# Performance work log

Hardware: AMD Instinct MI355X
Metric: run time of the kernel (lower is better)

Reference implementation:

```python
import jax, jax.numpy as jnp
import numpy as np

N_HASHES = 4
CHUNK = 144
REDUCTION = 4
RES_SCALE = 1.0
NORM_EPS = 5e-5


def conv2d(x, w, b, pad):
    y = jax.lax.conv_general_dilated(
        x, w, window_strides=(1, 1), padding=[(pad, pad), (pad, pad)],
        dimension_numbers=('NCHW', 'OIHW', 'NCHW'))
    return y + b[None, :, None, None]


def add_adjacent_buckets(x):
    # x: (N, h, n_chunks, chunk, e); concat each chunk with its circular neighbors
    back = jnp.roll(x, 1, axis=2)
    fwd = jnp.roll(x, -1, axis=2)
    return jnp.concatenate([x, back, fwd], axis=3)


def setup_inputs() -> dict:
    key = jax.random.key(0)
    ks = jax.random.split(key, 6)
    x = jax.random.normal(ks[0], (1, 32, 192, 192), jnp.float32)
    w_match = jax.random.normal(ks[1], (8, 32, 3, 3), jnp.float32) * 0.05
    b_match = jnp.zeros((8,), jnp.float32)
    w_asm = jax.random.normal(ks[2], (32, 32, 1, 1), jnp.float32) * 0.05
    b_asm = jnp.zeros((32,), jnp.float32)
    rotations = jax.random.normal(ks[3], (8, N_HASHES, 64), jnp.float32)
    return {'x': x, 'w_match': w_match, 'b_match': b_match,
            'w_asm': w_asm, 'b_asm': b_asm, 'rotations': rotations}


def reference(x, w_match, b_match, w_asm, b_asm, rotations):
    N, _, H, W = x.shape
    L = H * W
    # conv_match: 3x3 conv 32->8; conv_assembly: 1x1 conv 32->32
    x_embed = conv2d(x, w_match, b_match, 1).reshape(N, -1, L).transpose(0, 2, 1)  # (N, L, 8)
    y_embed = conv2d(x, w_asm, b_asm, 0).reshape(N, -1, L).transpose(0, 2, 1)      # (N, L, 32)
    C = x_embed.shape[-1]
    hash_buckets = min(L // CHUNK + (L // CHUNK) % 2, 128)  # = 128 here

    # --- LSH hashing (non-differentiable; rotations passed in for determinism) ---
    rotated = jnp.einsum('blf,fhi->bhli', x_embed, rotations)        # (N, h, L, hb/2)
    rotated = jnp.concatenate([rotated, -rotated], axis=-1)          # (N, h, L, hb)
    hash_codes = jnp.argmax(rotated, axis=-1)                        # (N, h, L)
    hash_codes = hash_codes + (jnp.arange(N_HASHES) * hash_buckets)[None, :, None]
    hash_codes = hash_codes.reshape(N, -1)                           # (N, h*L)

    # --- sort tokens by bucket id ---
    indices = jnp.argsort(hash_codes, axis=-1)
    undo_sort = jnp.argsort(indices, axis=-1)
    mod_indices = indices % L
    x_sorted = jnp.take_along_axis(x_embed, mod_indices[:, :, None], axis=1)  # (N, h*L, 8)
    y_sorted = jnp.take_along_axis(y_embed, mod_indices[:, :, None], axis=1)  # (N, h*L, 32)

    x_b = x_sorted.reshape(N, N_HASHES, -1, C)
    y_b = y_sorted.reshape(N, N_HASHES, -1, C * REDUCTION)
    padding = (-L) % CHUNK  # static; 0 for L=192*192
    if padding:
        x_b = jnp.concatenate([x_b, x_b[:, :, -padding:, :]], axis=2)
        y_b = jnp.concatenate([y_b, y_b[:, :, -padding:, :]], axis=2)
    x_b = x_b.reshape(N, N_HASHES, -1, CHUNK, C)
    y_b = y_b.reshape(N, N_HASHES, -1, CHUNK, C * REDUCTION)

    # --- bucketed attention with adjacent buckets ---
    nrm = jnp.linalg.norm(x_b, axis=-1, keepdims=True)
    x_match = x_b / jnp.maximum(nrm, NORM_EPS)   # F.normalize(eps=5e-5)
    x_match = add_adjacent_buckets(x_match)      # (N, h, k, 3*chunk, 8)
    y_adj = add_adjacent_buckets(y_b)            # (N, h, k, 3*chunk, 32)

    raw = jnp.einsum('bhkie,bhkje->bhkij', x_b, x_match)  # (N, h, k, 144, 432)
    bucket_score = jax.scipy.special.logsumexp(raw, axis=-1, keepdims=True)
    score = jnp.exp(raw - bucket_score)
    ret = jnp.einsum('bhkij,bhkje->bhkie', score, y_adj)  # (N, h, k, 144, 32)

    ret = ret.reshape(N, N_HASHES, -1, C * REDUCTION)
    bucket_score = bucket_score.reshape(N, N_HASHES, -1)
    if padding:
        ret = ret[:, :, :-padding, :]
        bucket_score = bucket_score[:, :, :-padding]
    ret = ret.reshape(N, -1, C * REDUCTION)
    bucket_score = bucket_score.reshape(N, -1)

    # --- unsort and combine hash rounds via softmax over logsumexp scores ---
    ret = jnp.take_along_axis(ret, undo_sort[:, :, None], axis=1)
    bucket_score = jnp.take_along_axis(bucket_score, undo_sort, axis=1)
    ret = ret.reshape(N, N_HASHES, L, C * REDUCTION)
    probs = jax.nn.softmax(bucket_score.reshape(N, N_HASHES, L, 1), axis=1)
    out = jnp.sum(ret * probs, axis=1)                     # (N, L, 32)
    out = out.transpose(0, 2, 1).reshape(N, -1, H, W) * RES_SCALE + x
    return out
```

## Files before the change

### kernel.cpp

```cpp
#include <hip/hip_runtime.h>
#include <hip/hip_bf16.h>
#include <math.h>

#define LTOT 36864
#define NH 4
#define NCHUNK 256
#define CHU 144
#define NBUCK 128
#define NSEG 144
#define HW_ 192
#define VTS 148

typedef unsigned int u32;
typedef unsigned short u16;
typedef unsigned long long u64;
typedef __attribute__((ext_vector_type(4))) short short4v;
typedef __attribute__((ext_vector_type(4))) float f32x4;

__device__ __forceinline__ u32 pkbf(float a, float b){
  union { __hip_bfloat162 h2; u32 u; } cv;
  cv.h2 = __float22bfloat162_rn(float2{a,b});
  return cv.u;
}
__device__ __forceinline__ float bflo(u32 w){ return __uint_as_float(w<<16); }
__device__ __forceinline__ float bfhi(u32 w){ return __uint_as_float(w & 0xffff0000u); }

__global__ __launch_bounds__(256) void k_conv(const float* __restrict__ x,
    const float* __restrict__ wm, const float* __restrict__ bm,
    const float* __restrict__ wa, const float* __restrict__ ba,
    float* __restrict__ xe, u16* __restrict__ Vu)
{
  __shared__ float xs[32*108];
  const int t = threadIdx.x;
  const int id = blockIdx.x;
  const int bx = id % 12, by = id / 12;

  for (int idx=t; idx<3456; idx+=256){
    int ci = idx/108, rem = idx-ci*108;
    int iy = rem/18,  ix = rem-iy*18;
    int yy = by*4+iy-1, xx = bx*16+ix-1;
    float v = 0.f;
    if (yy>=0 && yy<HW_ && xx>=0 && xx<HW_) v = x[ci*LTOT + yy*HW_ + xx];
    xs[idx] = v;
  }
  __syncthreads();
  const int lane = t & 63;
  const int w  = __builtin_amdgcn_readfirstlane(t>>6);
  const int co0 = 2*w, cb = 8*w;
  const int ix = lane & 15, iy = lane >> 4;
  float a0 = bm[co0], a1 = bm[co0+1];
  float acc[8];
  #pragma unroll
  for (int co=0;co<8;co++) acc[co] = ba[cb+co];
  const float* xb  = xs + iy*18 + ix;
  const float* w0p = wm + co0*288;
  const float* w1p = w0p + 288;
  for (int ci=0; ci<32; ci++){
    const float* xp = xb + ci*108;
    float x00=xp[0],  x01=xp[1],  x02=xp[2];
    float x10=xp[18], x11=xp[19], x12=xp[20];
    float x20=xp[36], x21=xp[37], x22=xp[38];
    const float* w0 = w0p + ci*9;
    const float* w1 = w1p + ci*9;
    a0 += x00*w0[0]+x01*w0[1]+x02*w0[2]
        + x10*w0[3]+x11*w0[4]+x12*w0[5]
        + x20*w0[6]+x21*w0[7]+x22*w0[8];
    a1 += x00*w1[0]+x01*w1[1]+x02*w1[2]
        + x10*w1[3]+x11*w1[4]+x12*w1[5]
        + x20*w1[6]+x21*w1[7]+x22*w1[8];
    const float* wap = wa + cb*32 + ci;
    #pragma unroll
    for (int co=0;co<8;co++) acc[co] += x11 * wap[co*32];
  }
  const int l = (by*4+iy)*HW_ + bx*16+ix;
  *(float2*)(xe + l*8 + co0) = float2{a0,a1};
  uint4 vv;
  vv.x = pkbf(acc[0],acc[1]); vv.y = pkbf(acc[2],acc[3]);
  vv.z = pkbf(acc[4],acc[5]); vv.w = pkbf(acc[6],acc[7]);
  *(uint4*)(Vu + (size_t)l*32 + cb) = vv;
}

__global__ __launch_bounds__(256) void k_hashrank(const float* __restrict__ xe,
    const float* __restrict__ rot, int* __restrict__ code,
    int* __restrict__ lrank, int* __restrict__ hist)
{
  const int h = blockIdx.y, seg = blockIdx.x, t = threadIdx.x;
  const int l = seg*256 + t;
  const float4* qp = (const float4*)(xe + l*8);
  float4 qa = qp[0], qb = qp[1];
  float best = -INFINITY; int bi = 0;
  float worst = INFINITY; int wi = 0;
  for (int i=0; i<64; i++){
    const float* rp = rot + h*64 + i;
    float v = qa.x*rp[0]    + qa.y*rp[256]  + qa.z*rp[512]  + qa.w*rp[768]
            + qb.x*rp[1024] + qb.y*rp[1280] + qb.z*rp[1536] + qb.w*rp[1792];
    if (v > best)  { best  = v; bi = i; }
    if (v < worst) { worst = v; wi = i; }
  }
  int c = (-worst > best) ? (64+wi) : bi;
  code[h*LTOT + l] = c;

  const int lane = t & 63, w = t >> 6;
  u64 mask = ~0ull;
  #pragma unroll
  for (int bit=0; bit<7; bit++){
    u64 bset = __ballot((c>>bit)&1);
    mask &= ((c>>bit)&1) ? bset : ~bset;
  }
  int rin = __popcll(mask & ((lane==0)?0ull:(~0ull >> (64-lane))));
  int cnt = __popcll(mask);

  __shared__ int wh[4][NBUCK];
  ((int*)wh)[t] = 0; ((int*)wh)[t+256] = 0;
  __syncthreads();
  if (rin == 0) wh[w][c] = cnt;
  __syncthreads();
  int r = rin;
  for (int ww=0; ww<w; ww++) r += wh[ww][c];
  lrank[h*LTOT + l] = r;
  if (t < NBUCK) hist[(h*NSEG+seg)*NBUCK + t] = wh[0][t]+wh[1][t]+wh[2][t]+wh[3][t];
}

__global__ __launch_bounds__(512) void k_scan(const int* __restrict__ hist,
    int* __restrict__ segoff)
{
  const int h = blockIdx.x;
  const int b = threadIdx.x & 127, g = threadIdx.x >> 7;
  int vals[36];
  int sum = 0;
  #pragma unroll
  for (int i=0;i<36;i++){
    vals[i] = hist[(h*NSEG + g*36 + i)*NBUCK + b];
    sum += vals[i];
  }
  __shared__ int ps[4][NBUCK];
  __shared__ int tot[NBUCK];
  __shared__ int scv[NBUCK];
  ps[g][b] = sum;
  __syncthreads();
  if (g == 0){
    int run = 0;
    #pragma unroll
    for (int gg=0; gg<4; gg++){ int tv = ps[gg][b]; ps[gg][b] = run; run += tv; }
    tot[b] = run;
    int v = run;
    #pragma unroll
    for (int off=1; off<64; off<<=1){
      int u = __shfl_up(v, off);
      if ((b & 63) >= off) v += u;
    }
    scv[b] = v;
  }
  __syncthreads();
  int base = scv[b] - tot[b] + ((b >= 64) ? scv[63] : 0);
  int run2 = base + ps[g][b];
  #pragma unroll
  for (int i=0;i<36;i++){
    segoff[(h*NSEG + g*36 + i)*NBUCK + b] = run2;
    run2 += vals[i];
  }
}

__global__ __launch_bounds__(256) void k_scatter(const int* __restrict__ code,
    const int* __restrict__ lrank, const int* __restrict__ segoff,
    const float* __restrict__ xe, const u16* __restrict__ Vu,
    int* __restrict__ spos, u16* __restrict__ Ks, u16* __restrict__ Qs,
    u16* __restrict__ Vs)
{
  const int h = blockIdx.y, seg = blockIdx.x, t = threadIdx.x;
  const int l = seg*256 + t;
  int c = code[h*LTOT + l];
  int r = segoff[(h*NSEG+seg)*NBUCK + c] + lrank[h*LTOT + l];
  spos[h*LTOT + r] = l;

  const float4* xr = (const float4*)(xe + l*8);
  float4 a = xr[0], b = xr[1];
  float n2 = a.x*a.x+a.y*a.y+a.z*a.z+a.w*a.w
           + b.x*b.x+b.y*b.y+b.z*b.z+b.w*b.w;
  float sc = 1.0f / fmaxf(sqrtf(n2), 5e-5f);
  uint4 kk, qq;
  kk.x = pkbf(a.x*sc,a.y*sc); kk.y = pkbf(a.z*sc,a.w*sc);
  kk.z = pkbf(b.x*sc,b.y*sc); kk.w = pkbf(b.z*sc,b.w*sc);
  qq.x = pkbf(a.x,a.y); qq.y = pkbf(a.z,a.w);
  qq.z = pkbf(b.x,b.y); qq.w = pkbf(b.z,b.w);
  *(uint4*)(Ks + (size_t)(h*LTOT + r)*8) = kk;
  *(uint4*)(Qs + (size_t)(h*LTOT + r)*8) = qq;

  const uint4* vr = (const uint4*)(Vu + (size_t)l*32);
  uint4* vp = (uint4*)(Vs + (size_t)(h*LTOT + r)*32);
  vp[0] = vr[0]; vp[1] = vr[1]; vp[2] = vr[2]; vp[3] = vr[3];
}

__global__ __launch_bounds__(320) void k_attn(const u16* __restrict__ Ks,
    const u16* __restrict__ Qs, const u16* __restrict__ Vs,
    const int* __restrict__ spos, u16* __restrict__ ret_u, float* __restrict__ bs_u)
{
  __shared__ __align__(16) u16 Klds[CHU*8];
  __shared__ __align__(16) u16 Qlds[CHU*8];
  __shared__ __align__(16) u16 VT[32*VTS];
  __shared__ float qn[CHU];
  __shared__ int spos_l[CHU];

  const int t = threadIdx.x;
  const int k = blockIdx.x, h = blockIdx.y;

  if (t < CHU){
    uint4 qv = *(const uint4*)(Qs + (size_t)(h*LTOT + k*CHU + t)*8);
    *(uint4*)(Qlds + t*8) = qv;
    float f0=bflo(qv.x), f1=bfhi(qv.x), f2=bflo(qv.y), f3=bfhi(qv.y);
    float f4=bflo(qv.z), f5=bfhi(qv.z), f6=bflo(qv.w), f7=bfhi(qv.w);
    qn[t] = sqrtf(f0*f0+f1*f1+f2*f2+f3*f3+f4*f4+f5*f5+f6*f6+f7*f7)*1.01f + 1e-6f;
    spos_l[t] = spos[h*LTOT + k*CHU + t];
  }
  __syncthreads();

  const int lane = t & 63;
  const int wv = t >> 6;
  const int q = lane & 15;
  const int quad = lane >> 4;
  const bool two = (wv < 4);
  const int tl0 = 2*wv;
  const int tl1 = two ? (2*wv+1) : 8;

  const short4v zs = {0,0,0,0};
  short4v bq0 = zs, bq1 = zs;
  if (quad < 2){
    bq0 = *(const short4v*)(Qlds + (tl0*16+q)*8 + quad*4);
    if (two) bq1 = *(const short4v*)(Qlds + (tl1*16+q)*8 + quad*4);
  }
  const float m0 = qn[tl0*16+q];
  const float m1 = two ? qn[tl1*16+q] : 0.f;

  f32x4 o00={0,0,0,0}, o01={0,0,0,0}, o10={0,0,0,0}, o11={0,0,0,0};
  float s0 = 0.f, s1 = 0.f;

  for (int r=0; r<3; r++){
    __syncthreads();
    const int gkb = ((k + NCHUNK-1 + r) & (NCHUNK-1)) * CHU;
    if (t < CHU){
      *(uint4*)(Klds + t*8) = *(const uint4*)(Ks + (size_t)(h*LTOT + gkb + t)*8);
    } else if (t >= 176){
      int i = t - 176;
      int p = i >> 1, hf = i & 1;
      const uint4* ra = (const uint4*)(Vs + (size_t)(h*LTOT + gkb + 2*p)*32);
      const uint4* rb = (const uint4*)(Vs + (size_t)(h*LTOT + gkb + 2*p+1)*32);
      uint4 A0 = ra[hf*2], A1 = ra[hf*2+1];
      uint4 B0 = rb[hf*2], B1 = rb[hf*2+1];
      u32 aw[8] = {A0.x,A0.y,A0.z,A0.w,A1.x,A1.y,A1.z,A1.w};
      u32 bw[8] = {B0.x,B0.y,B0.z,B0.w,B1.x,B1.y,B1.z,B1.w};
      int ebase = hf*16;
      #pragma unroll
      for (int m=0;m<8;m++){
        u32 al = aw[m]&0xffffu, ah = aw[m]>>16;
        u32 bl = bw[m]&0xffffu, bh = bw[m]>>16;
        *(u32*)&VT[(ebase+2*m  )*VTS + 2*p] = al | (bl<<16);
        *(u32*)&VT[(ebase+2*m+1)*VTS + 2*p] = ah | (bh<<16);
      }
    }
    __syncthreads();

    #pragma unroll 3
    for (int kt=0; kt<9; kt++){
      short4v av = zs;
      if (quad < 2) av = *(const short4v*)(Klds + (kt*16+q)*8 + quad*4);
      f32x4 zc = {0.f,0.f,0.f,0.f};
      f32x4 stA = __builtin_amdgcn_mfma_f32_16x16x16bf16_1k(av, bq0, zc, 0,0,0);

      float pA0 = __expf(stA[0]-m0), pA1 = __expf(stA[1]-m0);
      float pA2 = __expf(stA[2]-m0), pA3 = __expf(stA[3]-m0);
      s0 += (pA0+pA1)+(pA2+pA3);
      union { u32 u[2]; short4v s4; } pkA;
      pkA.u[0] = pkbf(pA0,pA1); pkA.u[1] = pkbf(pA2,pA3);

      short4v va0 = *(const short4v*)(&VT[ q    *VTS + kt*16 + quad*4]);
      short4v va1 = *(const short4v*)(&VT[(q+16)*VTS + kt*16 + quad*4]);
      o00 = __builtin_amdgcn_mfma_f32_16x16x16bf16_1k(va0, pkA.s4, o00, 0,0,0);
      o01 = __builtin_amdgcn_mfma_f32_16x16x16bf16_1k(va1, pkA.s4, o01, 0,0,0);

      if (two){
        f32x4 stB = __builtin_amdgcn_mfma_f32_16x16x16bf16_1k(av, bq1, zc, 0,0,0);
        float pB0 = __expf(stB[0]-m1), pB1 = __expf(stB[1]-m1);
        float pB2 = __expf(stB[2]-m1), pB3 = __expf(stB[3]-m1);
        s1 += (pB0+pB1)+(pB2+pB3);
        union { u32 u[2]; short4v s4; } pkB;
        pkB.u[0] = pkbf(pB0,pB1); pkB.u[1] = pkbf(pB2,pB3);
        o10 = __builtin_amdgcn_mfma_f32_16x16x16bf16_1k(va0, pkB.s4, o10, 0,0,0);
        o11 = __builtin_amdgcn_mfma_f32_16x16x16bf16_1k(va1, pkB.s4, o11, 0,0,0);
      }
    }
  }

  float st0 = s0;
  st0 += __shfl_xor(st0, 16); st0 += __shfl_xor(st0, 32);
  float inv0 = 1.0f/st0;

  const int pos0 = spos_l[tl0*16 + q];
  u16* rp0 = ret_u + (size_t)(h*LTOT + pos0)*32;
  uint2 wA, wB;
  wA.x = pkbf(o00[0]*inv0, o00[1]*inv0); wA.y = pkbf(o00[2]*inv0, o00[3]*inv0);
  wB.x = pkbf(o01[0]*inv0, o01[1]*inv0); wB.y = pkbf(o01[2]*inv0, o01[3]*inv0);
  *(uint2*)&rp0[quad*4]    = wA;
  *(uint2*)&rp0[16+quad*4] = wB;
  if (quad == 0) bs_u[h*LTOT + pos0] = m0 + __logf(st0);

  if (two){
    float st1 = s1;
    st1 += __shfl_xor(st1, 16); st1 += __shfl_xor(st1, 32);
    float inv1 = 1.0f/st1;
    const int pos1 = spos_l[tl1*16 + q];
    u16* rp1 = ret_u + (size_t)(h*LTOT + pos1)*32;
    wA.x = pkbf(o10[0]*inv1, o10[1]*inv1); wA.y = pkbf(o10[2]*inv1, o10[3]*inv1);
    wB.x = pkbf(o11[0]*inv1, o11[1]*inv1); wB.y = pkbf(o11[2]*inv1, o11[3]*inv1);
    *(uint2*)&rp1[quad*4]    = wA;
    *(uint2*)&rp1[16+quad*4] = wB;
    if (quad == 0) bs_u[h*LTOT + pos1] = m1 + __logf(st1);
  }
}

__global__ __launch_bounds__(256) void k_final(const float* __restrict__ x,
    const u16* __restrict__ ret_u, const float* __restrict__ bs_u,
    float* __restrict__ out)
{
  const int l  = blockIdx.x*64 + (threadIdx.x & 63);
  const int eg = threadIdx.x >> 6;
  float bs[NH];
  #pragma unroll
  for (int h=0;h<NH;h++) bs[h] = bs_u[h*LTOT + l];
  float m = fmaxf(fmaxf(bs[0],bs[1]), fmaxf(bs[2],bs[3]));
  float p[NH]; float s = 0.f;
  #pragma unroll
  for (int h=0;h<NH;h++){ p[h] = __expf(bs[h]-m); s += p[h]; }
  float inv = 1.0f/s;
  float o[8];
  #pragma unroll
  for (int e=0;e<8;e++) o[e]=0.f;
  #pragma unroll
  for (int h=0;h<NH;h++){
    float w = p[h]*inv;
    uint4 v = *(const uint4*)(ret_u + (size_t)(h*LTOT + l)*32 + eg*8);
    o[0] += w*bflo(v.x); o[1] += w*bfhi(v.x);
    o[2] += w*bflo(v.y); o[3] += w*bfhi(v.y);
    o[4] += w*bflo(v.z); o[5] += w*bfhi(v.z);
    o[6] += w*bflo(v.w); o[7] += w*bfhi(v.w);
  }
  #pragma unroll
  for (int e=0;e<8;e++){
    int ge = eg*8 + e;
    out[ge*LTOT + l] = o[e] + x[ge*LTOT + l];
  }
}

extern "C" void kernel_launch(void* const* d_in, const int* in_sizes, int n_in,
                              void* d_out, int out_size, void* d_ws, size_t ws_size,
                              hipStream_t stream)
{
  const float* x   = (const float*)d_in[0];
  const float* wm  = (const float*)d_in[1];
  const float* bm  = (const float*)d_in[2];
  const float* wa  = (const float*)d_in[3];
  const float* ba  = (const float*)d_in[4];
  const float* rot = (const float*)d_in[5];
  float* out = (float*)d_out;

  char* ws = (char*)d_ws;
  size_t off = 0;
  auto alloc = [&](size_t bytes)->void*{
    void* p = ws + off;
    off = (off + bytes + 255) & ~(size_t)255;
    return p;
  };
  float* xe     = (float*)alloc((size_t)LTOT*8*4);
  u16*   Vu     = (u16*)  alloc((size_t)LTOT*32*2);
  int*   code   = (int*)  alloc((size_t)NH*LTOT*4);
  int*   lrank  = (int*)  alloc((size_t)NH*LTOT*4);
  int*   hist   = (int*)  alloc((size_t)NH*NSEG*NBUCK*4);
  int*   segoff = (int*)  alloc((size_t)NH*NSEG*NBUCK*4);
  int*   spos   = (int*)  alloc((size_t)NH*LTOT*4);
  u16*   Ks     = (u16*)  alloc((size_t)NH*LTOT*8*2);
  u16*   Qs     = (u16*)  alloc((size_t)NH*LTOT*8*2);
  u16*   Vs     = (u16*)  alloc((size_t)NH*LTOT*32*2);
  u16*   ret_u  = (u16*)  alloc((size_t)NH*LTOT*32*2);
  float* bs_u   = (float*)alloc((size_t)NH*LTOT*4);

  hipLaunchKernelGGL(k_conv,     dim3(576),        dim3(256), 0, stream, x, wm, bm, wa, ba, xe, Vu);
  hipLaunchKernelGGL(k_hashrank, dim3(NSEG,NH),    dim3(256), 0, stream, xe, rot, code, lrank, hist);
  hipLaunchKernelGGL(k_scan,     dim3(NH),         dim3(512), 0, stream, hist, segoff);
  hipLaunchKernelGGL(k_scatter,  dim3(NSEG,NH),    dim3(256), 0, stream, code, lrank, segoff, xe, Vu, spos, Ks, Qs, Vs);
  hipLaunchKernelGGL(k_attn,     dim3(NCHUNK,NH),  dim3(320), 0, stream, Ks, Qs, Vs, spos, ret_u, bs_u);
  hipLaunchKernelGGL(k_final,    dim3(576),        dim3(256), 0, stream, x, ret_u, bs_u, out);
}
```

Measured before the change: 130.5 us.

## Preload all neighbour K chunks and double-buffer V with register prefetch

All three adjacent K chunks are now loaded into a larger shared buffer once at kernel start, so K no longer has to be reloaded each round. V tiles use two shared buffers: the next chunk's V is fetched into registers before the MFMA loop and transposed into the other buffer afterwards. This drops from two barriers per round to one and overlaps global V loads with compute. The cost is more shared memory and extra live registers for the prefetched V. A stray no-op read-modify-write on VT remains in the prologue.

```diff
diff --git a/kernel.cpp b/kernel.cpp
--- a/kernel.cpp
+++ b/kernel.cpp
@@ -195,14 +195,17 @@
     const u16* __restrict__ Qs, const u16* __restrict__ Vs,
     const int* __restrict__ spos, u16* __restrict__ ret_u, float* __restrict__ bs_u)
 {
-  __shared__ __align__(16) u16 Klds[CHU*8];
+  __shared__ __align__(16) u16 Klds[432*8];
   __shared__ __align__(16) u16 Qlds[CHU*8];
-  __shared__ __align__(16) u16 VT[32*VTS];
+  __shared__ __align__(16) u16 VT[2][32*VTS];
   __shared__ float qn[CHU];
   __shared__ int spos_l[CHU];
 
   const int t = threadIdx.x;
   const int k = blockIdx.x, h = blockIdx.y;
+  const int vp_i = t - 176, vp_p = vp_i >> 1, vp_hf = vp_i & 1;
+
+  uint4 vpa0, vpa1, vpb0, vpb1;
 
   if (t < CHU){
     uint4 qv = *(const uint4*)(Qs + (size_t)(h*LTOT + k*CHU + t)*8);
@@ -211,6 +214,31 @@
     float f4=bflo(qv.z), f5=bfhi(qv.z), f6=bflo(qv.w), f7=bfhi(qv.w);
     qn[t] = sqrtf(f0*f0+f1*f1+f2*f2+f3*f3+f4*f4+f5*f5+f6*f6+f7*f7)*1.01f + 1e-6f;
     spos_l[t] = spos[h*LTOT + k*CHU + t];
+    #pragma unroll
+    for (int rr=0; rr<3; rr++){
+      const int gkb = ((k + NCHUNK-1 + rr) & (NCHUNK-1)) * CHU;
+      *(uint4*)(Klds + (rr*CHU + t)*8) =
+          *(const uint4*)(Ks + (size_t)(h*LTOT + gkb + t)*8);
+    }
+  } else if (t >= 176){
+    const int gkb = ((k + NCHUNK-1) & (NCHUNK-1)) * CHU;
+    const uint4* ra = (const uint4*)(Vs + (size_t)(h*LTOT + gkb + 2*vp_p)*32);
+    const uint4* rb = (const uint4*)(Vs + (size_t)(h*LTOT + gkb + 2*vp_p+1)*32);
+    vpa0 = ra[vp_hf*2]; vpa1 = ra[vp_hf*2+1];
+    vpb0 = rb[vp_hf*2]; vpb1 = rb[vp_hf*2+1];
+  }
+  if (t >= 176){
+    u32 aw[8] = {vpa0.x,vpa0.y,vpa0.z,vpa0.w,vpa1.x,vpa1.y,vpa1.z,vpa1.w};
+    u32 bw[8] = {vpb0.x,vpb0.y,vpb0.z,vpb0.w,vpb1.x,vpb1.y,vpb1.z,vpb1.w};
+    int ebase = vp_hf*16;
+    #pragma unroll
+    for (int m=0;m<8;m++){
+      u32 al = aw[m]&0xffffu, ah = aw[m]>>16;
+      u32 bl = bw[m]&0xffffu, bh = bw[m]>>16;
+      VT[0][(ebase+2*m  )*VTS + 2*vp_p] |= 0;
+      *(u32*)&VT[0][(ebase+2*m  )*VTS + 2*vp_p] = al | (bl<<16);
+      *(u32*)&VT[0][(ebase+2*m+1)*VTS + 2*vp_p] = ah | (bh<<16);
+    }
   }
   __syncthreads();
 
@@ -235,34 +263,19 @@
   float s0 = 0.f, s1 = 0.f;
 
   for (int r=0; r<3; r++){
-    __syncthreads();
-    const int gkb = ((k + NCHUNK-1 + r) & (NCHUNK-1)) * CHU;
-    if (t < CHU){
-      *(uint4*)(Klds + t*8) = *(const uint4*)(Ks + (size_t)(h*LTOT + gkb + t)*8);
-    } else if (t >= 176){
-      int i = t - 176;
-      int p = i >> 1, hf = i & 1;
-      const uint4* ra = (const uint4*)(Vs + (size_t)(h*LTOT + gkb + 2*p)*32);
-      const uint4* rb = (const uint4*)(Vs + (size_t)(h*LTOT + gkb + 2*p+1)*32);
-      uint4 A0 = ra[hf*2], A1 = ra[hf*2+1];
-      uint4 B0 = rb[hf*2], B1 = rb[hf*2+1];
-      u32 aw[8] = {A0.x,A0.y,A0.z,A0.w,A1.x,A1.y,A1.z,A1.w};
-      u32 bw[8] = {B0.x,B0.y,B0.z,B0.w,B1.x,B1.y,B1.z,B1.w};
-      int ebase = hf*16;
-      #pragma unroll
-      for (int m=0;m<8;m++){
-        u32 al = aw[m]&0xffffu, ah = aw[m]>>16;
-        u32 bl = bw[m]&0xffffu, bh = bw[m]>>16;
-        *(u32*)&VT[(ebase+2*m  )*VTS + 2*p] = al | (bl<<16);
-        *(u32*)&VT[(ebase+2*m+1)*VTS + 2*p] = ah | (bh<<16);
-      }
-    }
-    __syncthreads();
+    if (r < 2 && t >= 176){
+      const int gkb = ((k + NCHUNK + r) & (NCHUNK-1)) * CHU;
+      const uint4* ra = (const uint4*)(Vs + (size_t)(h*LTOT + gkb + 2*vp_p)*32);
+      const uint4* rb = (const uint4*)(Vs + (size_t)(h*LTOT + gkb + 2*vp_p+1)*32);
+      vpa0 = ra[vp_hf*2]; vpa1 = ra[vp_hf*2+1];
+      vpb0 = rb[vp_hf*2]; vpb1 = rb[vp_hf*2+1];
+    }
+    const u16* vtb = VT[r & 1];
 
     #pragma unroll 3
     for (int kt=0; kt<9; kt++){
       short4v av = zs;
-      if (quad < 2) av = *(const short4v*)(Klds + (kt*16+q)*8 + quad*4);
+      if (quad < 2) av = *(const short4v*)(Klds + ((r*9+kt)*16+q)*8 + quad*4);
       f32x4 zc = {0.f,0.f,0.f,0.f};
       f32x4 stA = __builtin_amdgcn_mfma_f32_16x16x16bf16_1k(av, bq0, zc, 0,0,0);
 
@@ -272,8 +285,8 @@
       union { u32 u[2]; short4v s4; } pkA;
       pkA.u[0] = pkbf(pA0,pA1); pkA.u[1] = pkbf(pA2,pA3);
 
-      short4v va0 = *(const short4v*)(&VT[ q    *VTS + kt*16 + quad*4]);
-      short4v va1 = *(const short4v*)(&VT[(q+16)*VTS + kt*16 + quad*4]);
+      short4v va0 = *(const short4v*)(&vtb[ q    *VTS + kt*16 + quad*4]);
+      short4v va1 = *(const short4v*)(&vtb[(q+16)*VTS + kt*16 + quad*4]);
       o00 = __builtin_amdgcn_mfma_f32_16x16x16bf16_1k(va0, pkA.s4, o00, 0,0,0);
       o01 = __builtin_amdgcn_mfma_f32_16x16x16bf16_1k(va1, pkA.s4, o01, 0,0,0);
 
@@ -287,6 +300,23 @@
         o10 = __builtin_amdgcn_mfma_f32_16x16x16bf16_1k(va0, pkB.s4, o10, 0,0,0);
         o11 = __builtin_amdgcn_mfma_f32_16x16x16bf16_1k(va1, pkB.s4, o11, 0,0,0);
       }
+    }
+
+    if (r < 2){
+      if (t >= 176){
+        u32 aw[8] = {vpa0.x,vpa0.y,vpa0.z,vpa0.w,vpa1.x,vpa1.y,vpa1.z,vpa1.w};
+        u32 bw[8] = {vpb0.x,vpb0.y,vpb0.z,vpb0.w,vpb1.x,vpb1.y,vpb1.z,vpb1.w};
+        int ebase = vp_hf*16;
+        u16* vtn = (u16*)VT[(r+1) & 1];
+        #pragma unroll
+        for (int m=0;m<8;m++){
+          u32 al = aw[m]&0xffffu, ah = aw[m]>>16;
+          u32 bl = bw[m]&0xffffu, bh = bw[m]>>16;
+          *(u32*)&vtn[(ebase+2*m  )*VTS + 2*vp_p] = al | (bl<<16);
+          *(u32*)&vtn[(ebase+2*m+1)*VTS + 2*vp_p] = ah | (bh<<16);
+        }
+      }
+      __syncthreads();
     }
   }
 
```

Result: no change. 130.0 us (-0.4%).

## Fuse hash-code computation into conv and stage all neighbor chunks once in attention

Applied to the files above, without the earlier changes.

Hash-code argmax computation moves from the separate hashrank kernel into the conv kernel, where each of the 4 waves computes one hash round from embeddings staged in shared memory. The ranking part stays in a new k_rank kernel that reads the stored codes. The attention kernel now loads K and the transposed V for all three adjacent chunks up front into larger LDS buffers, then runs one 27-tile loop. This removes the per-round barriers and reloads. The cost is more LDS per block, which may lower occupancy.

```diff
diff --git a/kernel.cpp b/kernel.cpp
--- a/kernel.cpp
+++ b/kernel.cpp
@@ -28,9 +28,11 @@
 __global__ __launch_bounds__(256) void k_conv(const float* __restrict__ x,
     const float* __restrict__ wm, const float* __restrict__ bm,
     const float* __restrict__ wa, const float* __restrict__ ba,
-    float* __restrict__ xe, u16* __restrict__ Vu)
+    const float* __restrict__ rot,
+    float* __restrict__ xe, u16* __restrict__ Vu, int* __restrict__ code)
 {
   __shared__ float xs[32*108];
+  __shared__ float xq[64*8];
   const int t = threadIdx.x;
   const int id = blockIdx.x;
   const int bx = id % 12, by = id / 12;
@@ -74,19 +76,15 @@
   }
   const int l = (by*4+iy)*HW_ + bx*16+ix;
   *(float2*)(xe + l*8 + co0) = float2{a0,a1};
+  *(float2*)(xq + lane*8 + co0) = float2{a0,a1};
   uint4 vv;
   vv.x = pkbf(acc[0],acc[1]); vv.y = pkbf(acc[2],acc[3]);
   vv.z = pkbf(acc[4],acc[5]); vv.w = pkbf(acc[6],acc[7]);
   *(uint4*)(Vu + (size_t)l*32 + cb) = vv;
-}
-
-__global__ __launch_bounds__(256) void k_hashrank(const float* __restrict__ xe,
-    const float* __restrict__ rot, int* __restrict__ code,
-    int* __restrict__ lrank, int* __restrict__ hist)
-{
-  const int h = blockIdx.y, seg = blockIdx.x, t = threadIdx.x;
-  const int l = seg*256 + t;
-  const float4* qp = (const float4*)(xe + l*8);
+  __syncthreads();
+
+  const int h = w;
+  const float4* qp = (const float4*)(xq + lane*8);
   float4 qa = qp[0], qb = qp[1];
   float best = -INFINITY; int bi = 0;
   float worst = INFINITY; int wi = 0;
@@ -98,7 +96,16 @@
     if (v < worst) { worst = v; wi = i; }
   }
   int c = (-worst > best) ? (64+wi) : bi;
-  code[h*LTOT + l] = c;
+  const int ly = lane >> 4, lx = lane & 15;
+  code[h*LTOT + (by*4+ly)*HW_ + bx*16+lx] = c;
+}
+
+__global__ __launch_bounds__(256) void k_rank(const int* __restrict__ code,
+    int* __restrict__ lrank, int* __restrict__ hist)
+{
+  const int h = blockIdx.y, seg = blockIdx.x, t = threadIdx.x;
+  const int l = seg*256 + t;
+  int c = code[h*LTOT + l];
 
   const int lane = t & 63, w = t >> 6;
   u64 mask = ~0ull;
@@ -195,9 +202,9 @@
     const u16* __restrict__ Qs, const u16* __restrict__ Vs,
     const int* __restrict__ spos, u16* __restrict__ ret_u, float* __restrict__ bs_u)
 {
-  __shared__ __align__(16) u16 Klds[CHU*8];
+  __shared__ __align__(16) u16 Klds[432*8];
   __shared__ __align__(16) u16 Qlds[CHU*8];
-  __shared__ __align__(16) u16 VT[32*VTS];
+  __shared__ __align__(16) u16 VT[3][32*VTS];
   __shared__ float qn[CHU];
   __shared__ int spos_l[CHU];
 
@@ -211,6 +218,33 @@
     float f4=bflo(qv.z), f5=bfhi(qv.z), f6=bflo(qv.w), f7=bfhi(qv.w);
     qn[t] = sqrtf(f0*f0+f1*f1+f2*f2+f3*f3+f4*f4+f5*f5+f6*f6+f7*f7)*1.01f + 1e-6f;
     spos_l[t] = spos[h*LTOT + k*CHU + t];
+    #pragma unroll
+    for (int rr=0; rr<3; rr++){
+      const int gkb = ((k + NCHUNK-1 + rr) & (NCHUNK-1)) * CHU;
+      *(uint4*)(Klds + (rr*CHU + t)*8) =
+          *(const uint4*)(Ks + (size_t)(h*LTOT + gkb + t)*8);
+    }
+  }
+  for (int j = t; j < 432; j += 320){
+    int p = j >> 1, hf = j & 1;
+    int g = 2*p;
+    int rg = g / CHU, lk = g - rg*CHU;
+    const int gkb = ((k + NCHUNK-1 + rg) & (NCHUNK-1)) * CHU;
+    const uint4* ra = (const uint4*)(Vs + (size_t)(h*LTOT + gkb + lk)*32);
+    const uint4* rb = (const uint4*)(Vs + (size_t)(h*LTOT + gkb + lk+1)*32);
+    uint4 A0 = ra[hf*2], A1 = ra[hf*2+1];
+    uint4 B0 = rb[hf*2], B1 = rb[hf*2+1];
+    u32 aw[8] = {A0.x,A0.y,A0.z,A0.w,A1.x,A1.y,A1.z,A1.w};
+    u32 bw[8] = {B0.x,B0.y,B0.z,B0.w,B1.x,B1.y,B1.z,B1.w};
+    int ebase = hf*16;
+    u16* vtb = (u16*)VT[rg];
+    #pragma unroll
+    for (int m=0;m<8;m++){
+      u32 al = aw[m]&0xffffu, ah = aw[m]>>16;
+      u32 bl = bw[m]&0xffffu, bh = bw[m]>>16;
+      *(u32*)&vtb[(ebase+2*m  )*VTS + lk] = al | (bl<<16);
+      *(u32*)&vtb[(ebase+2*m+1)*VTS + lk] = ah | (bh<<16);
+    }
   }
   __syncthreads();
 
@@ -234,59 +268,35 @@
   f32x4 o00={0,0,0,0}, o01={0,0,0,0}, o10={0,0,0,0}, o11={0,0,0,0};
   float s0 = 0.f, s1 = 0.f;
 
-  for (int r=0; r<3; r++){
-    __syncthreads();
-    const int gkb = ((k + NCHUNK-1 + r) & (NCHUNK-1)) * CHU;
-    if (t < CHU){
-      *(uint4*)(Klds + t*8) = *(const uint4*)(Ks + (size_t)(h*LTOT + gkb + t)*8);
-    } else if (t >= 176){
-      int i = t - 176;
-      int p = i >> 1, hf = i & 1;
-      const uint4* ra = (const uint4*)(Vs + (size_t)(h*LTOT + gkb + 2*p)*32);
-      const uint4* rb = (const uint4*)(Vs + (size_t)(h*LTOT + gkb + 2*p+1)*32);
-      uint4 A0 = ra[hf*2], A1 = ra[hf*2+1];
-      uint4 B0 = rb[hf*2], B1 = rb[hf*2+1];
-      u32 aw[8] = {A0.x,A0.y,A0.z,A0.w,A1.x,A1.y,A1.z,A1.w};
-      u32 bw[8] = {B0.x,B0.y,B0.z,B0.w,B1.x,B1.y,B1.z,B1.w};
-      int ebase = hf*16;
-      #pragma unroll
-      for (int m=0;m<8;m++){
-        u32 al = aw[m]&0xffffu, ah = aw[m]>>16;
-        u32 bl = bw[m]&0xffffu, bh = bw[m]>>16;
-        *(u32*)&VT[(ebase+2*m  )*VTS + 2*p] = al | (bl<<16);
-        *(u32*)&VT[(ebase+2*m+1)*VTS + 2*p] = ah | (bh<<16);
-      }
-    }
-    __syncthreads();
-
-    #pragma unroll 3
-    for (int kt=0; kt<9; kt++){
-      short4v av = zs;
-      if (quad < 2) av = *(const short4v*)(Klds + (kt*16+q)*8 + quad*4);
-      f32x4 zc = {0.f,0.f,0.f,0.f};
-      f32x4 stA = __builtin_amdgcn_mfma_f32_16x16x16bf16_1k(av, bq0, zc, 0,0,0);
-
-      float pA0 = __expf(stA[0]-m0), pA1 = __expf(stA[1]-m0);
-      float pA2 = __expf(stA[2]-m0), pA3 = __expf(stA[3]-m0);
-      s0 += (pA0+pA1)+(pA2+pA3);
-      union { u32 u[2]; short4v s4; } pkA;
-      pkA.u[0] = pkbf(pA0,pA1); pkA.u[1] = pkbf(pA2,pA3);
-
-      short4v va0 = *(const short4v*)(&VT[ q    *VTS + kt*16 + quad*4]);
-      short4v va1 = *(const short4v*)(&VT[(q+16)*VTS + kt*16 + quad*4]);
-      o00 = __builtin_amdgcn_mfma_f32_16x16x16bf16_1k(va0, pkA.s4, o00, 0,0,0);
-      o01 = __builtin_amdgcn_mfma_f32_16x16x16bf16_1k(va1, pkA.s4, o01, 0,0,0);
-
-      if (two){
-        f32x4 stB = __builtin_amdgcn_mfma_f32_16x16x16bf16_1k(av, bq1, zc, 0,0,0);
-        float pB0 = __expf(stB[0]-m1), pB1 = __expf(stB[1]-m1);
-        float pB2 = __expf(stB[2]-m1), pB3 = __expf(stB[3]-m1);
-        s1 += (pB0+pB1)+(pB2+pB3);
-        union { u32 u[2]; short4v s4; } pkB;
-        pkB.u[0] = pkbf(pB0,pB1); pkB.u[1] = pkbf(pB2,pB3);
-        o10 = __builtin_amdgcn_mfma_f32_16x16x16bf16_1k(va0, pkB.s4, o10, 0,0,0);
-        o11 = __builtin_amdgcn_mfma_f32_16x16x16bf16_1k(va1, pkB.s4, o11, 0,0,0);
-      }
+  #pragma unroll 3
+  for (int kt=0; kt<27; kt++){
+    const int rg = kt / 9, ktl = kt - rg*9;
+    const u16* vtb = VT[rg];
+    short4v av = zs;
+    if (quad < 2) av = *(const short4v*)(Klds + (kt*16+q)*8 + quad*4);
+    f32x4 zc = {0.f,0.f,0.f,0.f};
+    f32x4 stA = __builtin_amdgcn_mfma_f32_16x16x16bf16_1k(av, bq0, zc, 0,0,0);
+
+    float pA0 = __expf(stA[0]-m0), pA1 = __expf(stA[1]-m0);
+    float pA2 = __expf(stA[2]-m0), pA3 = __expf(stA[3]-m0);
+    s0 += (pA0+pA1)+(pA2+pA3);
+    union { u32 u[2]; short4v s4; } pkA;
+    pkA.u[0] = pkbf(pA0,pA1); pkA.u[1] = pkbf(pA2,pA3);
+
+    short4v va0 = *(const short4v*)(&vtb[ q    *VTS + ktl*16 + quad*4]);
+    short4v va1 = *(const short4v*)(&vtb[(q+16)*VTS + ktl*16 + quad*4]);
+    o00 = __builtin_amdgcn_mfma_f32_16x16x16bf16_1k(va0, pkA.s4, o00, 0,0,0);
+    o01 = __builtin_amdgcn_mfma_f32_16x16x16bf16_1k(va1, pkA.s4, o01, 0,0,0);
+
+    if (two){
+      f32x4 stB = __builtin_amdgcn_mfma_f32_16x16x16bf16_1k(av, bq1, zc, 0,0,0);
+      float pB0 = __expf(stB[0]-m1), pB1 = __expf(stB[1]-m1);
+      float pB2 = __expf(stB[2]-m1), pB3 = __expf(stB[3]-m1);
+      s1 += (pB0+pB1)+(pB2+pB3);
+      union { u32 u[2]; short4v s4; } pkB;
+      pkB.u[0] = pkbf(pB0,pB1); pkB.u[1] = pkbf(pB2,pB3);
+      o10 = __builtin_amdgcn_mfma_f32_16x16x16bf16_1k(va0, pkB.s4, o10, 0,0,0);
+      o11 = __builtin_amdgcn_mfma_f32_16x16x16bf16_1k(va1, pkB.s4, o11, 0,0,0);
     }
   }
 
@@ -382,10 +392,10 @@
   u16*   ret_u  = (u16*)  alloc((size_t)NH*LTOT*32*2);
   float* bs_u   = (float*)alloc((size_t)NH*LTOT*4);
 
-  hipLaunchKernelGGL(k_conv,     dim3(576),        dim3(256), 0, stream, x, wm, bm, wa, ba, xe, Vu);
-  hipLaunchKernelGGL(k_hashrank, dim3(NSEG,NH),    dim3(256), 0, stream, xe, rot, code, lrank, hist);
-  hipLaunchKernelGGL(k_scan,     dim3(NH),         dim3(512), 0, stream, hist, segoff);
-  hipLaunchKernelGGL(k_scatter,  dim3(NSEG,NH),    dim3(256), 0, stream, code, lrank, segoff, xe, Vu, spos, Ks, Qs, Vs);
-  hipLaunchKernelGGL(k_attn,     dim3(NCHUNK,NH),  dim3(320), 0, stream, Ks, Qs, Vs, spos, ret_u, bs_u);
-  hipLaunchKernelGGL(k_final,    dim3(576),        dim3(256), 0, stream, x, ret_u, bs_u, out);
-}
+  hipLaunchKernelGGL(k_conv,    dim3(576),        dim3(256), 0, stream, x, wm, bm, wa, ba, rot, xe, Vu, code);
+  hipLaunchKernelGGL(k_rank,    dim3(NSEG,NH),    dim3(256), 0, stream, code, lrank, hist);
+  hipLaunchKernelGGL(k_scan,    dim3(NH),         dim3(512), 0, stream, hist, segoff);
+  hipLaunchKernelGGL(k_scatter, dim3(NSEG,NH),    dim3(256), 0, stream, code, lrank, segoff, xe, Vu, spos, Ks, Qs, Vs);
+  hipLaunchKernelGGL(k_attn,    dim3(NCHUNK,NH),  dim3(320), 0, stream, Ks, Qs, Vs, spos, ret_u, bs_u);
+  hipLaunchKernelGGL(k_final,   dim3(576),        dim3(256), 0, stream, x, ret_u, bs_u, out);
+}
```

New measurement: 130.3 us. About the same (-0.2%).

## Fuse hashing into conv, fold scan into scatter, split attention across neighbor chunks

Applied to the files above, without the earlier changes.

Hash-code computation moves into the conv kernel, with a global atomic histogram replacing the separate hashrank kernel. The per-segment prefix scan is recomputed inside each scatter block, which drops the k_scan launch and the lrank/segoff buffers. Attention now splits its three adjacent-chunk passes across a third grid dimension. Each block writes unnormalized partial outputs and partial sums that k_final combines using a shared per-row max. This triples attention parallelism and removes two launches, at the cost of redundant hist reads in scatter, atomics, a memset, and three times the partial-output traffic.

```diff
diff --git a/kernel.cpp b/kernel.cpp
--- a/kernel.cpp
+++ b/kernel.cpp
@@ -28,9 +28,12 @@
 __global__ __launch_bounds__(256) void k_conv(const float* __restrict__ x,
     const float* __restrict__ wm, const float* __restrict__ bm,
     const float* __restrict__ wa, const float* __restrict__ ba,
-    float* __restrict__ xe, u16* __restrict__ Vu)
+    const float* __restrict__ rot,
+    float* __restrict__ xe, u16* __restrict__ Vu, int* __restrict__ code,
+    int* __restrict__ hist)
 {
   __shared__ float xs[32*108];
+  __shared__ float xq[64*8];
   const int t = threadIdx.x;
   const int id = blockIdx.x;
   const int bx = id % 12, by = id / 12;
@@ -74,19 +77,15 @@
   }
   const int l = (by*4+iy)*HW_ + bx*16+ix;
   *(float2*)(xe + l*8 + co0) = float2{a0,a1};
+  *(float2*)(xq + lane*8 + co0) = float2{a0,a1};
   uint4 vv;
   vv.x = pkbf(acc[0],acc[1]); vv.y = pkbf(acc[2],acc[3]);
   vv.z = pkbf(acc[4],acc[5]); vv.w = pkbf(acc[6],acc[7]);
   *(uint4*)(Vu + (size_t)l*32 + cb) = vv;
-}
-
-__global__ __launch_bounds__(256) void k_hashrank(const float* __restrict__ xe,
-    const float* __restrict__ rot, int* __restrict__ code,
-    int* __restrict__ lrank, int* __restrict__ hist)
-{
-  const int h = blockIdx.y, seg = blockIdx.x, t = threadIdx.x;
-  const int l = seg*256 + t;
-  const float4* qp = (const float4*)(xe + l*8);
+  __syncthreads();
+
+  const int h = w;
+  const float4* qp = (const float4*)(xq + lane*8);
   float4 qa = qp[0], qb = qp[1];
   float best = -INFINITY; int bi = 0;
   float worst = INFINITY; int wi = 0;
@@ -98,8 +97,38 @@
     if (v < worst) { worst = v; wi = i; }
   }
   int c = (-worst > best) ? (64+wi) : bi;
-  code[h*LTOT + l] = c;
-
+  const int ly = lane >> 4, lx = lane & 15;
+  const int lpix = (by*4+ly)*HW_ + bx*16+lx;
+  code[h*LTOT + lpix] = c;
+  atomicAdd(&hist[(h*NSEG + (lpix>>8))*NBUCK + c], 1);
+}
+
+__global__ __launch_bounds__(256) void k_scatter(const int* __restrict__ code,
+    const int* __restrict__ hist,
+    const float* __restrict__ xe, const u16* __restrict__ Vu,
+    int* __restrict__ spos, u16* __restrict__ Ks, u16* __restrict__ Qs,
+    u16* __restrict__ Vs)
+{
+  const int h = blockIdx.y, seg = blockIdx.x, t = threadIdx.x;
+  const int l = seg*256 + t;
+  int c = code[h*LTOT + l];
+
+  __shared__ int pre2[2][NBUCK], tot2[2][NBUCK];
+  __shared__ int scv[NBUCK];
+  __shared__ int segbase[NBUCK];
+  __shared__ int wh[4][NBUCK];
+
+  {
+    const int b = t & 127, gg = t >> 7;
+    int pre = 0, tt = 0;
+    const int sA = gg*72;
+    for (int s = sA; s < sA+72; s++){
+      int v = hist[(h*NSEG+s)*NBUCK + b];
+      tt += v;
+      if (s < seg) pre += v;
+    }
+    pre2[gg][b] = pre; tot2[gg][b] = tt;
+  }
   const int lane = t & 63, w = t >> 6;
   u64 mask = ~0ull;
   #pragma unroll
@@ -109,68 +138,31 @@
   }
   int rin = __popcll(mask & ((lane==0)?0ull:(~0ull >> (64-lane))));
   int cnt = __popcll(mask);
-
-  __shared__ int wh[4][NBUCK];
   ((int*)wh)[t] = 0; ((int*)wh)[t+256] = 0;
   __syncthreads();
+
   if (rin == 0) wh[w][c] = cnt;
-  __syncthreads();
-  int r = rin;
-  for (int ww=0; ww<w; ww++) r += wh[ww][c];
-  lrank[h*LTOT + l] = r;
-  if (t < NBUCK) hist[(h*NSEG+seg)*NBUCK + t] = wh[0][t]+wh[1][t]+wh[2][t]+wh[3][t];
-}
-
-__global__ __launch_bounds__(512) void k_scan(const int* __restrict__ hist,
-    int* __restrict__ segoff)
-{
-  const int h = blockIdx.x;
-  const int b = threadIdx.x & 127, g = threadIdx.x >> 7;
-  int vals[36];
-  int sum = 0;
-  #pragma unroll
-  for (int i=0;i<36;i++){
-    vals[i] = hist[(h*NSEG + g*36 + i)*NBUCK + b];
-    sum += vals[i];
-  }
-  __shared__ int ps[4][NBUCK];
-  __shared__ int tot[NBUCK];
-  __shared__ int scv[NBUCK];
-  ps[g][b] = sum;
-  __syncthreads();
-  if (g == 0){
-    int run = 0;
-    #pragma unroll
-    for (int gg=0; gg<4; gg++){ int tv = ps[gg][b]; ps[gg][b] = run; run += tv; }
-    tot[b] = run;
-    int v = run;
+  if (t < NBUCK){
+    int tt = tot2[0][t] + tot2[1][t];
+    int v = tt;
     #pragma unroll
     for (int off=1; off<64; off<<=1){
       int u = __shfl_up(v, off);
-      if ((b & 63) >= off) v += u;
-    }
-    scv[b] = v;
-  }
-  __syncthreads();
-  int base = scv[b] - tot[b] + ((b >= 64) ? scv[63] : 0);
-  int run2 = base + ps[g][b];
-  #pragma unroll
-  for (int i=0;i<36;i++){
-    segoff[(h*NSEG + g*36 + i)*NBUCK + b] = run2;
-    run2 += vals[i];
-  }
-}
-
-__global__ __launch_bounds__(256) void k_scatter(const int* __restrict__ code,
-    const int* __restrict__ lrank, const int* __restrict__ segoff,
-    const float* __restrict__ xe, const u16* __restrict__ Vu,
-    int* __restrict__ spos, u16* __restrict__ Ks, u16* __restrict__ Qs,
-    u16* __restrict__ Vs)
-{
-  const int h = blockIdx.y, seg = blockIdx.x, t = threadIdx.x;
-  const int l = seg*256 + t;
-  int c = code[h*LTOT + l];
-  int r = segoff[(h*NSEG+seg)*NBUCK + c] + lrank[h*LTOT + l];
+      if ((t & 63) >= off) v += u;
+    }
+    scv[t] = v;
+  }
+  __syncthreads();
+
+  if (t < NBUCK){
+    int tt = tot2[0][t] + tot2[1][t];
+    int excl = scv[t] - tt + ((t >= 64) ? scv[63] : 0);
+    segbase[t] = excl + pre2[0][t] + pre2[1][t];
+  }
+  __syncthreads();
+
+  int r = segbase[c] + rin;
+  for (int ww=0; ww<w; ww++) r += wh[ww][c];
   spos[h*LTOT + r] = l;
 
   const float4* xr = (const float4*)(xe + l*8);
@@ -193,7 +185,8 @@
 
 __global__ __launch_bounds__(320) void k_attn(const u16* __restrict__ Ks,
     const u16* __restrict__ Qs, const u16* __restrict__ Vs,
-    const int* __restrict__ spos, u16* __restrict__ ret_u, float* __restrict__ bs_u)
+    const int* __restrict__ spos, u16* __restrict__ retp,
+    float* __restrict__ sp, float* __restrict__ bmx)
 {
   __shared__ __align__(16) u16 Klds[CHU*8];
   __shared__ __align__(16) u16 Qlds[CHU*8];
@@ -202,7 +195,8 @@
   __shared__ int spos_l[CHU];
 
   const int t = threadIdx.x;
-  const int k = blockIdx.x, h = blockIdx.y;
+  const int k = blockIdx.x, h = blockIdx.y, rg = blockIdx.z;
+  const int gkb = ((k + NCHUNK-1 + rg) & (NCHUNK-1)) * CHU;
 
   if (t < CHU){
     uint4 qv = *(const uint4*)(Qs + (size_t)(h*LTOT + k*CHU + t)*8);
@@ -211,6 +205,24 @@
     float f4=bflo(qv.z), f5=bfhi(qv.z), f6=bflo(qv.w), f7=bfhi(qv.w);
     qn[t] = sqrtf(f0*f0+f1*f1+f2*f2+f3*f3+f4*f4+f5*f5+f6*f6+f7*f7)*1.01f + 1e-6f;
     spos_l[t] = spos[h*LTOT + k*CHU + t];
+    *(uint4*)(Klds + t*8) = *(const uint4*)(Ks + (size_t)(h*LTOT + gkb + t)*8);
+  } else if (t >= 176){
+    int i = t - 176;
+    int p = i >> 1, hf = i & 1;
+    const uint4* ra = (const uint4*)(Vs + (size_t)(h*LTOT + gkb + 2*p)*32);
+    const uint4* rb = (const uint4*)(Vs + (size_t)(h*LTOT + gkb + 2*p+1)*32);
+    uint4 A0 = ra[hf*2], A1 = ra[hf*2+1];
+    uint4 B0 = rb[hf*2], B1 = rb[hf*2+1];
+    u32 aw[8] = {A0.x,A0.y,A0.z,A0.w,A1.x,A1.y,A1.z,A1.w};
+    u32 bw[8] = {B0.x,B0.y,B0.z,B0.w,B1.x,B1.y,B1.z,B1.w};
+    int ebase = hf*16;
+    #pragma unroll
+    for (int m=0;m<8;m++){
+      u32 al = aw[m]&0xffffu, ah = aw[m]>>16;
+      u32 bl = bw[m]&0xffffu, bh = bw[m]>>16;
+      *(u32*)&VT[(ebase+2*m  )*VTS + 2*p] = al | (bl<<16);
+      *(u32*)&VT[(ebase+2*m+1)*VTS + 2*p] = ah | (bh<<16);
+    }
   }
   __syncthreads();
 
@@ -234,114 +246,104 @@
   f32x4 o00={0,0,0,0}, o01={0,0,0,0}, o10={0,0,0,0}, o11={0,0,0,0};
   float s0 = 0.f, s1 = 0.f;
 
-  for (int r=0; r<3; r++){
-    __syncthreads();
-    const int gkb = ((k + NCHUNK-1 + r) & (NCHUNK-1)) * CHU;
-    if (t < CHU){
-      *(uint4*)(Klds + t*8) = *(const uint4*)(Ks + (size_t)(h*LTOT + gkb + t)*8);
-    } else if (t >= 176){
-      int i = t - 176;
-      int p = i >> 1, hf = i & 1;
-      const uint4* ra = (const uint4*)(Vs + (size_t)(h*LTOT + gkb + 2*p)*32);
-      const uint4* rb = (const uint4*)(Vs + (size_t)(h*LTOT + gkb + 2*p+1)*32);
-      uint4 A0 = ra[hf*2], A1 = ra[hf*2+1];
-      uint4 B0 = rb[hf*2], B1 = rb[hf*2+1];
-      u32 aw[8] = {A0.x,A0.y,A0.z,A0.w,A1.x,A1.y,A1.z,A1.w};
-      u32 bw[8] = {B0.x,B0.y,B0.z,B0.w,B1.x,B1.y,B1.z,B1.w};
-      int ebase = hf*16;
-      #pragma unroll
-      for (int m=0;m<8;m++){
-        u32 al = aw[m]&0xffffu, ah = aw[m]>>16;
-        u32 bl = bw[m]&0xffffu, bh = bw[m]>>16;
-        *(u32*)&VT[(ebase+2*m  )*VTS + 2*p] = al | (bl<<16);
-        *(u32*)&VT[(ebase+2*m+1)*VTS + 2*p] = ah | (bh<<16);
-      }
-    }
-    __syncthreads();
-
-    #pragma unroll 3
-    for (int kt=0; kt<9; kt++){
-      short4v av = zs;
-      if (quad < 2) av = *(const short4v*)(Klds + (kt*16+q)*8 + quad*4);
-      f32x4 zc = {0.f,0.f,0.f,0.f};
-      f32x4 stA = __builtin_amdgcn_mfma_f32_16x16x16bf16_1k(av, bq0, zc, 0,0,0);
-
-      float pA0 = __expf(stA[0]-m0), pA1 = __expf(stA[1]-m0);
-      float pA2 = __expf(stA[2]-m0), pA3 = __expf(stA[3]-m0);
-      s0 += (pA0+pA1)+(pA2+pA3);
-      union { u32 u[2]; short4v s4; } pkA;
-      pkA.u[0] = pkbf(pA0,pA1); pkA.u[1] = pkbf(pA2,pA3);
-
-      short4v va0 = *(const short4v*)(&VT[ q    *VTS + kt*16 + quad*4]);
-      short4v va1 = *(const short4v*)(&VT[(q+16)*VTS + kt*16 + quad*4]);
-      o00 = __builtin_amdgcn_mfma_f32_16x16x16bf16_1k(va0, pkA.s4, o00, 0,0,0);
-      o01 = __builtin_amdgcn_mfma_f32_16x16x16bf16_1k(va1, pkA.s4, o01, 0,0,0);
-
-      if (two){
-        f32x4 stB = __builtin_amdgcn_mfma_f32_16x16x16bf16_1k(av, bq1, zc, 0,0,0);
-        float pB0 = __expf(stB[0]-m1), pB1 = __expf(stB[1]-m1);
-        float pB2 = __expf(stB[2]-m1), pB3 = __expf(stB[3]-m1);
-        s1 += (pB0+pB1)+(pB2+pB3);
-        union { u32 u[2]; short4v s4; } pkB;
-        pkB.u[0] = pkbf(pB0,pB1); pkB.u[1] = pkbf(pB2,pB3);
-        o10 = __builtin_amdgcn_mfma_f32_16x16x16bf16_1k(va0, pkB.s4, o10, 0,0,0);
-        o11 = __builtin_amdgcn_mfma_f32_16x16x16bf16_1k(va1, pkB.s4, o11, 0,0,0);
-      }
+  #pragma unroll 3
+  for (int kt=0; kt<9; kt++){
+    short4v av = zs;
+    if (quad < 2) av = *(const short4v*)(Klds + (kt*16+q)*8 + quad*4);
+    f32x4 zc = {0.f,0.f,0.f,0.f};
+    f32x4 stA = __builtin_amdgcn_mfma_f32_16x16x16bf16_1k(av, bq0, zc, 0,0,0);
+
+    float pA0 = __expf(stA[0]-m0), pA1 = __expf(stA[1]-m0);
+    float pA2 = __expf(stA[2]-m0), pA3 = __expf(stA[3]-m0);
+    s0 += (pA0+pA1)+(pA2+pA3);
+    union { u32 u[2]; short4v s4; } pkA;
+    pkA.u[0] = pkbf(pA0,pA1); pkA.u[1] = pkbf(pA2,pA3);
+
+    short4v va0 = *(const short4v*)(&VT[ q    *VTS + kt*16 + quad*4]);
+    short4v va1 = *(const short4v*)(&VT[(q+16)*VTS + kt*16 + quad*4]);
+    o00 = __builtin_amdgcn_mfma_f32_16x16x16bf16_1k(va0, pkA.s4, o00, 0,0,0);
+    o01 = __builtin_amdgcn_mfma_f32_16x16x16bf16_1k(va1, pkA.s4, o01, 0,0,0);
+
+    if (two){
+      f32x4 stB = __builtin_amdgcn_mfma_f32_16x16x16bf16_1k(av, bq1, zc, 0,0,0);
+      float pB0 = __expf(stB[0]-m1), pB1 = __expf(stB[1]-m1);
+      float pB2 = __expf(stB[2]-m1), pB3 = __expf(stB[3]-m1);
+      s1 += (pB0+pB1)+(pB2+pB3);
+      union { u32 u[2]; short4v s4; } pkB;
+      pkB.u[0] = pkbf(pB0,pB1); pkB.u[1] = pkbf(pB2,pB3);
+      o10 = __builtin_amdgcn_mfma_f32_16x16x16bf16_1k(va0, pkB.s4, o10, 0,0,0);
+      o11 = __builtin_amdgcn_mfma_f32_16x16x16bf16_1k(va1, pkB.s4, o11, 0,0,0);
     }
   }
 
   float st0 = s0;
   st0 += __shfl_xor(st0, 16); st0 += __shfl_xor(st0, 32);
-  float inv0 = 1.0f/st0;
 
   const int pos0 = spos_l[tl0*16 + q];
-  u16* rp0 = ret_u + (size_t)(h*LTOT + pos0)*32;
+  u16* rp0 = retp + ((size_t)(rg*NH + h)*LTOT + pos0)*32;
   uint2 wA, wB;
-  wA.x = pkbf(o00[0]*inv0, o00[1]*inv0); wA.y = pkbf(o00[2]*inv0, o00[3]*inv0);
-  wB.x = pkbf(o01[0]*inv0, o01[1]*inv0); wB.y = pkbf(o01[2]*inv0, o01[3]*inv0);
+  wA.x = pkbf(o00[0], o00[1]); wA.y = pkbf(o00[2], o00[3]);
+  wB.x = pkbf(o01[0], o01[1]); wB.y = pkbf(o01[2], o01[3]);
   *(uint2*)&rp0[quad*4]    = wA;
   *(uint2*)&rp0[16+quad*4] = wB;
-  if (quad == 0) bs_u[h*LTOT + pos0] = m0 + __logf(st0);
+  if (quad == 0){
+    sp[(size_t)(rg*NH + h)*LTOT + pos0] = st0;
+    if (rg == 0) bmx[h*LTOT + pos0] = m0;
+  }
 
   if (two){
     float st1 = s1;
     st1 += __shfl_xor(st1, 16); st1 += __shfl_xor(st1, 32);
-    float inv1 = 1.0f/st1;
     const int pos1 = spos_l[tl1*16 + q];
-    u16* rp1 = ret_u + (size_t)(h*LTOT + pos1)*32;
-    wA.x = pkbf(o10[0]*inv1, o10[1]*inv1); wA.y = pkbf(o10[2]*inv1, o10[3]*inv1);
-    wB.x = pkbf(o11[0]*inv1, o11[1]*inv1); wB.y = pkbf(o11[2]*inv1, o11[3]*inv1);
+    u16* rp1 = retp + ((size_t)(rg*NH + h)*LTOT + pos1)*32;
+    wA.x = pkbf(o10[0], o10[1]); wA.y = pkbf(o10[2], o10[3]);
+    wB.x = pkbf(o11[0], o11[1]); wB.y = pkbf(o11[2], o11[3]);
     *(uint2*)&rp1[quad*4]    = wA;
     *(uint2*)&rp1[16+quad*4] = wB;
-    if (quad == 0) bs_u[h*LTOT + pos1] = m1 + __logf(st1);
+    if (quad == 0){
+      sp[(size_t)(rg*NH + h)*LTOT + pos1] = st1;
+      if (rg == 0) bmx[h*LTOT + pos1] = m1;
+    }
   }
 }
 
 __global__ __launch_bounds__(256) void k_final(const float* __restrict__ x,
-    const u16* __restrict__ ret_u, const float* __restrict__ bs_u,
-    float* __restrict__ out)
+    const u16* __restrict__ retp, const float* __restrict__ sp,
+    const float* __restrict__ bmx, float* __restrict__ out)
 {
   const int l  = blockIdx.x*64 + (threadIdx.x & 63);
   const int eg = threadIdx.x >> 6;
-  float bs[NH];
-  #pragma unroll
-  for (int h=0;h<NH;h++) bs[h] = bs_u[h*LTOT + l];
-  float m = fmaxf(fmaxf(bs[0],bs[1]), fmaxf(bs[2],bs[3]));
-  float p[NH]; float s = 0.f;
-  #pragma unroll
-  for (int h=0;h<NH;h++){ p[h] = __expf(bs[h]-m); s += p[h]; }
-  float inv = 1.0f/s;
+  float sh[NH], lse[NH];
+  #pragma unroll
+  for (int h=0;h<NH;h++){
+    float s = sp[(size_t)(0*NH+h)*LTOT + l]
+            + sp[(size_t)(1*NH+h)*LTOT + l]
+            + sp[(size_t)(2*NH+h)*LTOT + l];
+    sh[h] = s;
+    lse[h] = bmx[h*LTOT + l] + __logf(s);
+  }
+  float mm = fmaxf(fmaxf(lse[0],lse[1]), fmaxf(lse[2],lse[3]));
+  float p[NH]; float ssum = 0.f;
+  #pragma unroll
+  for (int h=0;h<NH;h++){ p[h] = __expf(lse[h]-mm); ssum += p[h]; }
+  float coef[NH];
+  #pragma unroll
+  for (int h=0;h<NH;h++) coef[h] = (p[h]/ssum) / sh[h];
+
   float o[8];
   #pragma unroll
   for (int e=0;e<8;e++) o[e]=0.f;
   #pragma unroll
-  for (int h=0;h<NH;h++){
-    float w = p[h]*inv;
-    uint4 v = *(const uint4*)(ret_u + (size_t)(h*LTOT + l)*32 + eg*8);
-    o[0] += w*bflo(v.x); o[1] += w*bfhi(v.x);
-    o[2] += w*bflo(v.y); o[3] += w*bfhi(v.y);
-    o[4] += w*bflo(v.z); o[5] += w*bfhi(v.z);
-    o[6] += w*bflo(v.w); o[7] += w*bfhi(v.w);
+  for (int rg=0;rg<3;rg++){
+    #pragma unroll
+    for (int h=0;h<NH;h++){
+      float w = coef[h];
+      uint4 v = *(const uint4*)(retp + ((size_t)(rg*NH+h)*LTOT + l)*32 + eg*8);
+      o[0] += w*bflo(v.x); o[1] += w*bfhi(v.x);
+      o[2] += w*bflo(v.y); o[3] += w*bfhi(v.y);
+      o[4] += w*bflo(v.z); o[5] += w*bfhi(v.z);
+      o[6] += w*bflo(v.w); o[7] += w*bfhi(v.w);
+    }
   }
   #pragma unroll
   for (int e=0;e<8;e++){
@@ -372,20 +374,18 @@
   float* xe     = (float*)alloc((size_t)LTOT*8*4);
   u16*   Vu     = (u16*)  alloc((size_t)LTOT*32*2);
   int*   code   = (int*)  alloc((size_t)NH*LTOT*4);
-  int*   lrank  = (int*)  alloc((size_t)NH*LTOT*4);
   int*   hist   = (int*)  alloc((size_t)NH*NSEG*NBUCK*4);
-  int*   segoff = (int*)  alloc((size_t)NH*NSEG*NBUCK*4);
   int*   spos   = (int*)  alloc((size_t)NH*LTOT*4);
   u16*   Ks     = (u16*)  alloc((size_t)NH*LTOT*8*2);
   u16*   Qs     = (u16*)  alloc((size_t)NH*LTOT*8*2);
   u16*   Vs     = (u16*)  alloc((size_t)NH*LTOT*32*2);
-  u16*   ret_u  = (u16*)  alloc((size_t)NH*LTOT*32*2);
-  float* bs_u   = (float*)alloc((size_t)NH*LTOT*4);
-
-  hipLaunchKernelGGL(k_conv,     dim3(576),        dim3(256), 0, stream, x, wm, bm, wa, ba, xe, Vu);
-  hipLaunchKernelGGL(k_hashrank, dim3(NSEG,NH),    dim3(256), 0, stream, xe, rot, code, lrank, hist);
-  hipLaunchKernelGGL(k_scan,     dim3(NH),         dim3(512), 0, stream, hist, segoff);
-  hipLaunchKernelGGL(k_scatter,  dim3(NSEG,NH),    dim3(256), 0, stream, code, lrank, segoff, xe, Vu, spos, Ks, Qs, Vs);
-  hipLaunchKernelGGL(k_attn,     dim3(NCHUNK,NH),  dim3(320), 0, stream, Ks, Qs, Vs, spos, ret_u, bs_u);
-  hipLaunchKernelGGL(k_final,    dim3(576),        dim3(256), 0, stream, x, ret_u, bs_u, out);
-}
+  u16*   retp   = (u16*)  alloc((size_t)3*NH*LTOT*32*2);
+  float* sp     = (float*)alloc((size_t)3*NH*LTOT*4);
+  float* bmx    = (float*)alloc((size_t)NH*LTOT*4);
+
+  hipMemsetAsync(hist, 0, (size_t)NH*NSEG*NBUCK*4, stream);
+  hipLaunchKernelGGL(k_conv,    dim3(576),          dim3(256), 0, stream, x, wm, bm, wa, ba, rot, xe, Vu, code, hist);
+  hipLaunchKernelGGL(k_scatter, dim3(NSEG,NH),      dim3(256), 0, stream, code, hist, xe, Vu, spos, Ks, Qs, Vs);
+  hipLaunchKernelGGL(k_attn,    dim3(NCHUNK,NH,3),  dim3(320), 0, stream, Ks, Qs, Vs, spos, retp, sp, bmx);
+  hipLaunchKernelGGL(k_final,   dim3(576),          dim3(256), 0, stream, x, retp, sp, bmx, out);
+}
```

New measurement: 132.1 us. Within noise of the previous version (+1.2%).
